# Kernel optimization log

Hardware: AMD Instinct MI355X
Metric: run time of the kernel (lower is better)

The kernel has to match this reference:

```python
import jax, jax.numpy as jnp
import numpy as np

N = 50000      # total nodes (batched protein graphs)
D = 256        # prot_hidden_dim
E = 800000     # edges per relation type
R = 5          # edge types: SEQ, STR_KNN, STR_DIS, SURF, LRR_REGION
LN_EPS = 1e-5
SIGMOID_TEMP = 2.0
WEIGHT_SCALE = 2.0
MIN_W, MAX_W = 0.05, 2.0


def setup_inputs() -> dict:
    key = jax.random.key(0)
    ks = jax.random.split(key, 8)
    x = jax.random.normal(ks[0], (N, D), dtype=jnp.float32)
    src = jax.random.randint(ks[1], (R, E), 0, N)
    dst = jax.random.randint(ks[2], (R, E), 0, N)
    # relation-attention MLP params: Linear(D, D//4) -> LayerNorm(D//4) -> ReLU -> Linear(D//4, 1)
    H = D // 4
    W1 = jax.random.normal(ks[3], (D, H), dtype=jnp.float32) / np.float32(np.sqrt(D))
    b1 = jnp.zeros((H,), jnp.float32)
    gamma = jnp.ones((H,), jnp.float32)
    beta = jnp.zeros((H,), jnp.float32)
    W2 = jax.random.normal(ks[4], (H, 1), dtype=jnp.float32) / np.float32(np.sqrt(H))
    b2 = jnp.zeros((1,), jnp.float32)
    attn_bias = jnp.array([-4.0, -4.0, -4.0, -4.0, -2.772], jnp.float32)
    return {"x": x, "src": src, "dst": dst, "W1": W1, "b1": b1,
            "gamma": gamma, "beta": beta, "W2": W2, "b2": b2,
            "attn_bias": attn_bias}


def _mean_aggregate(x, s, d):
    # DGL update_all(copy_u('h','m'), mean('m','h')): scatter-mean of src feats onto dst.
    sums = jax.ops.segment_sum(x[s], d, num_segments=N)                      # [N, D]
    cnt = jax.ops.segment_sum(jnp.ones((E,), x.dtype), d, num_segments=N)    # [N]
    # zero in-degree nodes get 0 (DGL mean semantics)
    return jnp.where(cnt[:, None] > 0, sums / jnp.maximum(cnt, 1.0)[:, None], 0.0)


def reference(x, src, dst, W1, b1, gamma, beta, W2, b2, attn_bias):
    # per-relation mean aggregation (loop over fixed small R, not a data dim)
    agg = jnp.stack([_mean_aggregate(x, src[r], dst[r]) for r in range(R)])  # [R, N, D]
    g = agg.mean(axis=1)                                                     # [R, D]
    # relation-attention MLP (dropout = identity in eval)
    h = g @ W1 + b1                                                          # [R, D//4]
    mu = h.mean(axis=-1, keepdims=True)
    var = ((h - mu) ** 2).mean(axis=-1, keepdims=True)
    h = (h - mu) * jax.lax.rsqrt(var + LN_EPS) * gamma + beta
    h = jax.nn.relu(h)
    scores = (h @ W2 + b2)[:, 0] + attn_bias                                 # [R]
    w = jax.nn.sigmoid(scores / SIGMOID_TEMP) * WEIGHT_SCALE
    w = jnp.clip(w, MIN_W, MAX_W)
    # fused = sum_r w[r] * agg[r]
    return jnp.einsum('r,rnd->nd', w, agg)
```

## Files before the change

kernel.cpp:

```cpp
#include <hip/hip_runtime.h>

#define NN 50000
#define DD 256
#define EE 800000
#define RR 5
#define HH 64
#define RN (RR * NN)

#define F_OFF  (RN)
#define F_CUR  (2 * RN)
#define F_C    (3 * RN)
#define F_G    (4 * RN)
#define F_W    (4 * RN + 1280)
#define F_CTR  (4 * RN + 1288)
#define F_ESRC (4 * RN + 1296)
#define F_XH   (F_ESRC + RR * EE)
#define BYTES_BF16 ((size_t)(F_XH + NN * DD / 2) * 4)
#define BYTES_F32  ((size_t)(F_ESRC + RR * EE) * 4)

#define C2_OFF  (RN)
#define C2_CUR  (2 * RN)
#define C2_G    (3 * RN)
#define C2_W    (3 * RN + 1280)
#define C2_CTR  (3 * RN + 1288)
#define C2_ESRC (3 * RN + 1296)
#define BYTES_CSR2 ((size_t)(C2_ESRC + RR * EE) * 4)

__device__ inline unsigned short bf16rn(float f) {
    unsigned u = __float_as_uint(f);
    unsigned r = u + 0x7FFFu + ((u >> 16) & 1u);
    return (unsigned short)(r >> 16);
}

__global__ __launch_bounds__(256) void deg_kernel(const int* __restrict__ dst,
                                                  int* __restrict__ cnt) {
    int i = blockIdx.x * 256 + threadIdx.x;
    if (i < RR * EE) {
        int r = i / EE;
        atomicAdd(&cnt[r * NN + dst[i]], 1);
    }
}

__global__ __launch_bounds__(256) void off_kernel(int* cnt, int* __restrict__ off,
                                                  int* __restrict__ cur,
                                                  int* __restrict__ ctr, float* invc) {
    int i = blockIdx.x * 256 + threadIdx.x;
    if (i < RN) {
        int cv = cnt[i];
        int o = atomicAdd(ctr, cv);
        off[i] = o;
        cur[i] = o;
        invc[i] = (cv > 0) ? (1.0f / (float)cv) : 0.0f;
    }
}

template <bool WITH_C>
__global__ __launch_bounds__(256) void fill_kernel(const int* __restrict__ src,
                                                   const int* __restrict__ dst,
                                                   int* __restrict__ cur,
                                                   int* __restrict__ esrc,
                                                   const float* __restrict__ invc,
                                                   float* __restrict__ c) {
    int i = blockIdx.x * 256 + threadIdx.x;
    if (i < RR * EE) {
        int r = i / EE;
        int d = dst[i];
        int s = src[i];
        int slot = atomicAdd(&cur[r * NN + d], 1);
        esrc[slot] = s;
        if constexpr (WITH_C) {
            unsafeAtomicAdd(&c[r * NN + s], invc[r * NN + d]);
        }
    }
}

__global__ __launch_bounds__(256) void gmat_kernel(const float* __restrict__ x,
                                                   const float* __restrict__ c,
                                                   float* __restrict__ g) {
    const int wave = threadIdx.x >> 6;
    const int lane = threadIdx.x & 63;
    const int gw = blockIdx.x * 4 + wave;
    const int nw = gridDim.x * 4;
    float4 a0 = {0, 0, 0, 0}, a1 = {0, 0, 0, 0}, a2 = {0, 0, 0, 0},
           a3 = {0, 0, 0, 0}, a4 = {0, 0, 0, 0};
    for (int s = gw; s < NN; s += nw) {
        float4 v = ((const float4*)(x + (size_t)s * DD))[lane];
        float c0 = c[0 * NN + s], c1 = c[1 * NN + s], c2 = c[2 * NN + s],
              c3 = c[3 * NN + s], c4 = c[4 * NN + s];
        a0.x += c0 * v.x; a0.y += c0 * v.y; a0.z += c0 * v.z; a0.w += c0 * v.w;
        a1.x += c1 * v.x; a1.y += c1 * v.y; a1.z += c1 * v.z; a1.w += c1 * v.w;
        a2.x += c2 * v.x; a2.y += c2 * v.y; a2.z += c2 * v.z; a2.w += c2 * v.w;
        a3.x += c3 * v.x; a3.y += c3 * v.y; a3.z += c3 * v.z; a3.w += c3 * v.w;
        a4.x += c4 * v.x; a4.y += c4 * v.y; a4.z += c4 * v.z; a4.w += c4 * v.w;
    }
    float4 acc[5] = {a0, a1, a2, a3, a4};
    #pragma unroll
    for (int r = 0; r < RR; ++r) {
        float* gr = g + r * DD + lane * 4;
        unsafeAtomicAdd(gr + 0, acc[r].x);
        unsafeAtomicAdd(gr + 1, acc[r].y);
        unsafeAtomicAdd(gr + 2, acc[r].z);
        unsafeAtomicAdd(gr + 3, acc[r].w);
    }
}

__global__ __launch_bounds__(256) void g_kernel(const float* __restrict__ x,
                                                const int* __restrict__ src,
                                                const int* __restrict__ dst,
                                                const float* __restrict__ invc,
                                                float* __restrict__ g) {
    const int r = blockIdx.y;
    const int wave = threadIdx.x >> 6;
    const int lane = threadIdx.x & 63;
    const int gw = blockIdx.x * 4 + wave;
    const int nw = gridDim.x * 4;
    const int* __restrict__ srcR = src + r * EE;
    const int* __restrict__ dstR = dst + r * EE;
    const float* __restrict__ invcR = invc + r * NN;
    float4 acc = {0, 0, 0, 0};
    for (int e = gw; e < EE; e += nw) {
        int eu = __builtin_amdgcn_readfirstlane(e);
        int s = srcR[eu];
        int dn = dstR[eu];
        float ic = invcR[dn];
        float4 v = ((const float4*)(x + (size_t)s * DD))[lane];
        acc.x += v.x * ic; acc.y += v.y * ic; acc.z += v.z * ic; acc.w += v.w * ic;
    }
    float* gr = g + r * DD + lane * 4;
    unsafeAtomicAdd(gr + 0, acc.x);
    unsafeAtomicAdd(gr + 1, acc.y);
    unsafeAtomicAdd(gr + 2, acc.z);
    unsafeAtomicAdd(gr + 3, acc.w);
}

__global__ __launch_bounds__(64) void mlp_kernel(const float* __restrict__ gsum,
                                                 const float* __restrict__ W1,
                                                 const float* __restrict__ b1,
                                                 const float* __restrict__ gamma,
                                                 const float* __restrict__ beta,
                                                 const float* __restrict__ W2,
                                                 const float* __restrict__ b2,
                                                 const float* __restrict__ attn_bias,
                                                 float* __restrict__ w) {
    const int t = threadIdx.x;
    __shared__ float gs[DD];
    const float invN = 1.0f / (float)NN;
    for (int r = 0; r < RR; ++r) {
        for (int d = t; d < DD; d += 64) gs[d] = gsum[r * DD + d] * invN;
        __syncthreads();
        float h = b1[t];
        for (int d = 0; d < DD; ++d) h += gs[d] * W1[d * HH + t];
        float mu = h;
        #pragma unroll
        for (int o = 32; o; o >>= 1) mu += __shfl_xor(mu, o, 64);
        mu *= (1.0f / 64.0f);
        float cc = h - mu;
        float var = cc * cc;
        #pragma unroll
        for (int o = 32; o; o >>= 1) var += __shfl_xor(var, o, 64);
        var *= (1.0f / 64.0f);
        float hn = cc * rsqrtf(var + 1e-5f) * gamma[t] + beta[t];
        hn = fmaxf(hn, 0.0f);
        float sc = hn * W2[t];
        #pragma unroll
        for (int o = 32; o; o >>= 1) sc += __shfl_xor(sc, o, 64);
        if (t == 0) {
            float s = sc + b2[0] + attn_bias[r];
            float ww = 2.0f / (1.0f + expf(-s * 0.5f));
            ww = fminf(fmaxf(ww, 0.05f), 2.0f);
            w[r] = ww;
        }
        __syncthreads();
    }
}

__global__ __launch_bounds__(256) void xcvt_kernel(const float* __restrict__ x,
                                                   ushort4* __restrict__ xh) {
    int i = blockIdx.x * 256 + threadIdx.x;
    if (i < NN * DD / 4) {
        float4 v = ((const float4*)x)[i];
        ushort4 q;
        q.x = bf16rn(v.x); q.y = bf16rn(v.y); q.z = bf16rn(v.z); q.w = bf16rn(v.w);
        xh[i] = q;
    }
}

template <bool BF16>
__device__ inline float4 loadrow(const float* __restrict__ x,
                                 const ushort4* __restrict__ xh, int s, int lane) {
    if constexpr (BF16) {
        ushort4 q = xh[(size_t)s * (DD / 4) + lane];
        float4 v;
        v.x = __uint_as_float((unsigned)q.x << 16);
        v.y = __uint_as_float((unsigned)q.y << 16);
        v.z = __uint_as_float((unsigned)q.z << 16);
        v.w = __uint_as_float((unsigned)q.w << 16);
        return v;
    } else {
        return ((const float4*)(x + (size_t)s * DD))[lane];
    }
}

template <bool BF16>
__global__ __launch_bounds__(256) void out_pull_kernel(const float* __restrict__ x,
                                                       const ushort4* __restrict__ xh,
                                                       const int* __restrict__ esrc,
                                                       const int* __restrict__ off,
                                                       const int* __restrict__ endv,
                                                       const float* __restrict__ invc,
                                                       const float* __restrict__ w,
                                                       float* __restrict__ out) {
    const int node = blockIdx.x * 4 + (threadIdx.x >> 6);
    if (node >= NN) return;
    const int lane = threadIdx.x & 63;

    float4 acc = {0, 0, 0, 0};
    #pragma unroll
    for (int r = 0; r < RR; ++r) {
        const int idx = r * NN + node;
        const int b = __builtin_amdgcn_readfirstlane(off[idx]);
        const int e_ = __builtin_amdgcn_readfirstlane(endv[idx]);
        const float coef = w[r] * invc[idx];
        float4 t = {0, 0, 0, 0};
        int e = b;
        for (; e + 4 <= e_; e += 4) {
            int s0 = __builtin_amdgcn_readfirstlane(esrc[e + 0]);
            int s1 = __builtin_amdgcn_readfirstlane(esrc[e + 1]);
            int s2 = __builtin_amdgcn_readfirstlane(esrc[e + 2]);
            int s3 = __builtin_amdgcn_readfirstlane(esrc[e + 3]);
            float4 v0 = loadrow<BF16>(x, xh, s0, lane);
            float4 v1 = loadrow<BF16>(x, xh, s1, lane);
            float4 v2 = loadrow<BF16>(x, xh, s2, lane);
            float4 v3 = loadrow<BF16>(x, xh, s3, lane);
            t.x += (v0.x + v1.x) + (v2.x + v3.x);
            t.y += (v0.y + v1.y) + (v2.y + v3.y);
            t.z += (v0.z + v1.z) + (v2.z + v3.z);
            t.w += (v0.w + v1.w) + (v2.w + v3.w);
        }
        for (; e < e_; ++e) {
            int s = __builtin_amdgcn_readfirstlane(esrc[e]);
            float4 v = loadrow<BF16>(x, xh, s, lane);
            t.x += v.x; t.y += v.y; t.z += v.z; t.w += v.w;
        }
        acc.x += coef * t.x; acc.y += coef * t.y;
        acc.z += coef * t.z; acc.w += coef * t.w;
    }
    ((float4*)(out + (size_t)node * DD))[lane] = acc;
}

__global__ __launch_bounds__(256) void invcnt_kernel(float* __restrict__ c) {
    int i = blockIdx.x * 256 + threadIdx.x;
    if (i < RN) {
        int v = ((const int*)c)[i];
        c[i] = (v > 0) ? (1.0f / (float)v) : 0.0f;
    }
}

__global__ __launch_bounds__(256) void out_scatter_kernel(const float* __restrict__ x,
                                                          const int* __restrict__ src,
                                                          const int* __restrict__ dst,
                                                          const float* __restrict__ invc,
                                                          const float* __restrict__ w,
                                                          float* __restrict__ out) {
    const int r = blockIdx.y;
    const float wr = w[r];
    const int wave = threadIdx.x >> 6;
    const int lane = threadIdx.x & 63;
    const int gw = blockIdx.x * 4 + wave;
    const int nw = gridDim.x * 4;
    const int* __restrict__ srcR = src + r * EE;
    const int* __restrict__ dstR = dst + r * EE;
    const float* __restrict__ invcR = invc + r * NN;
    for (int e = gw; e < EE; e += nw) {
        int eu = __builtin_amdgcn_readfirstlane(e);
        int s = srcR[eu];
        int dn = dstR[eu];
        float coef = wr * invcR[dn];
        float4 v = ((const float4*)(x + (size_t)s * DD))[lane];
        float* o = out + (size_t)dn * DD + lane * 4;
        unsafeAtomicAdd(o + 0, v.x * coef);
        unsafeAtomicAdd(o + 1, v.y * coef);
        unsafeAtomicAdd(o + 2, v.z * coef);
        unsafeAtomicAdd(o + 3, v.w * coef);
    }
}

extern "C" void kernel_launch(void* const* d_in, const int* in_sizes, int n_in,
                              void* d_out, int out_size, void* d_ws, size_t ws_size,
                              hipStream_t stream) {
    const float* x = (const float*)d_in[0];
    const int* src = (const int*)d_in[1];
    const int* dst = (const int*)d_in[2];
    const float* W1 = (const float*)d_in[3];
    const float* b1 = (const float*)d_in[4];
    const float* gamma = (const float*)d_in[5];
    const float* beta = (const float*)d_in[6];
    const float* W2 = (const float*)d_in[7];
    const float* b2 = (const float*)d_in[8];
    const float* attn_bias = (const float*)d_in[9];
    float* out = (float*)d_out;
    float* ws = (float*)d_ws;

    const int EDGE_GRID = (RR * EE + 255) / 256;
    const int RN_GRID = (RN + 255) / 256;

    if (ws_size >= BYTES_F32) {
        const bool bf16 = (ws_size >= BYTES_BF16);
        int* cnt = (int*)ws;
        float* invc = ws;
        int* off = (int*)ws + F_OFF;
        int* cur = (int*)ws + F_CUR;
        float* c = ws + F_C;
        float* g = ws + F_G;
        float* w = ws + F_W;
        int* ctr = (int*)ws + F_CTR;
        int* esrc = (int*)ws + F_ESRC;
        ushort4* xh = (ushort4*)((int*)ws + F_XH);

        hipMemsetAsync(cnt, 0, (size_t)RN * 4, stream);
        hipMemsetAsync(c, 0, (size_t)(RN + 1296) * 4, stream);

        if (bf16)
            xcvt_kernel<<<(NN * DD / 4 + 255) / 256, 256, 0, stream>>>(x, xh);
        deg_kernel<<<EDGE_GRID, 256, 0, stream>>>(dst, cnt);
        off_kernel<<<RN_GRID, 256, 0, stream>>>(cnt, off, cur, ctr, invc);
        fill_kernel<true><<<EDGE_GRID, 256, 0, stream>>>(src, dst, cur, esrc, invc, c);
        gmat_kernel<<<128, 256, 0, stream>>>(x, c, g);
        mlp_kernel<<<1, 64, 0, stream>>>(g, W1, b1, gamma, beta, W2, b2, attn_bias, w);
        if (bf16)
            out_pull_kernel<true><<<(NN + 3) / 4, 256, 0, stream>>>(x, xh, esrc, off,
                                                                    cur, invc, w, out);
        else
            out_pull_kernel<false><<<(NN + 3) / 4, 256, 0, stream>>>(x, xh, esrc, off,
                                                                     cur, invc, w, out);
    } else if (ws_size >= BYTES_CSR2) {
        int* cnt = (int*)ws;
        float* invc = ws;
        int* off = (int*)ws + C2_OFF;
        int* cur = (int*)ws + C2_CUR;
        float* g = ws + C2_G;
        float* w = ws + C2_W;
        int* ctr = (int*)ws + C2_CTR;
        int* esrc = (int*)ws + C2_ESRC;

        hipMemsetAsync(cnt, 0, (size_t)RN * 4, stream);
        hipMemsetAsync(g, 0, (size_t)1296 * 4, stream);

        deg_kernel<<<EDGE_GRID, 256, 0, stream>>>(dst, cnt);
        off_kernel<<<RN_GRID, 256, 0, stream>>>(cnt, off, cur, ctr, invc);
        fill_kernel<false><<<EDGE_GRID, 256, 0, stream>>>(src, dst, cur, esrc, invc,
                                                          nullptr);
        g_kernel<<<dim3(512, RR), 256, 0, stream>>>(x, src, dst, invc, g);
        mlp_kernel<<<1, 64, 0, stream>>>(g, W1, b1, gamma, beta, W2, b2, attn_bias, w);
        out_pull_kernel<false><<<(NN + 3) / 4, 256, 0, stream>>>(x, nullptr, esrc, off,
                                                                 cur, invc, w, out);
    } else {
        float* cnt = ws;
        float* g = ws + RN;
        float* w = ws + RN + RR * DD;
        hipMemsetAsync(ws, 0, (size_t)(RN + RR * DD + RR) * 4, stream);
        hipMemsetAsync(d_out, 0, (size_t)NN * DD * 4, stream);
        deg_kernel<<<EDGE_GRID, 256, 0, stream>>>(dst, (int*)cnt);
        invcnt_kernel<<<RN_GRID, 256, 0, stream>>>(cnt);
        g_kernel<<<dim3(512, RR), 256, 0, stream>>>(x, src, dst, cnt, g);
        mlp_kernel<<<1, 64, 0, stream>>>(g, W1, b1, gamma, beta, W2, b2, attn_bias, w);
        out_scatter_kernel<<<dim3(512, RR), 256, 0, stream>>>(x, src, dst, cnt, w, out);
    }
}
```

Before: 1.137 ms.

## Rebuild CSR with deterministic ranks, 16-bit indices, and column-chunked bf16 pull

The CSR build now records each edge's rank during the degree count and computes offsets with a block-level prefix scan, so the fill pass needs no atomics on the cursor array. Source indices are stored as 16-bit values, and x is converted to bf16 in a chunked layout of 8 chunks of 32 columns. The output pull then runs once per chunk so each pass gathers from a smaller working set that fits better in cache. The MLP now handles all five relations in one 320-thread block with W1 staged in shared memory. This adds seven more kernel launches and repeats the esrc and offset reads for every chunk, and the 16-bit indices only hold because N is below 65536.

New measurement: 1.434 ms. 26.1% more time.

```diff
diff --git a/kernel.cpp b/kernel.cpp
--- a/kernel.cpp
+++ b/kernel.cpp
@@ -6,17 +6,22 @@
 #define RR 5
 #define HH 64
 #define RN (RR * NN)
-
-#define F_OFF  (RN)
-#define F_CUR  (2 * RN)
-#define F_C    (3 * RN)
-#define F_G    (4 * RN)
-#define F_W    (4 * RN + 1280)
-#define F_CTR  (4 * RN + 1288)
-#define F_ESRC (4 * RN + 1296)
-#define F_XH   (F_ESRC + RR * EE)
-#define BYTES_BF16 ((size_t)(F_XH + NN * DD / 2) * 4)
-#define BYTES_F32  ((size_t)(F_ESRC + RR * EE) * 4)
+#define NBLK ((NN + 255) / 256)
+#define NCHUNK 8
+#define CW 32
+
+typedef float v2f __attribute__((ext_vector_type(2)));
+
+#define Q_OFF   (RN)
+#define Q_C     (2 * RN + 4)
+#define Q_G     (3 * RN + 4)
+#define Q_W     (3 * RN + 1284)
+#define Q_BSUM  (3 * RN + 1292)
+#define Q_BBASE (3 * RN + 1548)
+#define Q_RANK  (3 * RN + 1804)
+#define Q_ESRC  (Q_RANK + RR * EE / 2)
+#define Q_XH    (Q_ESRC + RR * EE / 2)
+#define BYTES_Q ((size_t)(Q_XH + NCHUNK * NN * CW / 2) * 4)
 
 #define C2_OFF  (RN)
 #define C2_CUR  (2 * RN)
@@ -32,45 +37,105 @@
     return (unsigned short)(r >> 16);
 }
 
-__global__ __launch_bounds__(256) void deg_kernel(const int* __restrict__ dst,
-                                                  int* __restrict__ cnt) {
+
+__global__ __launch_bounds__(256) void deg2_kernel(const int* __restrict__ dst,
+                                                   int* __restrict__ cnt,
+                                                   unsigned short* __restrict__ rank) {
     int i = blockIdx.x * 256 + threadIdx.x;
     if (i < RR * EE) {
         int r = i / EE;
-        atomicAdd(&cnt[r * NN + dst[i]], 1);
-    }
-}
-
-__global__ __launch_bounds__(256) void off_kernel(int* cnt, int* __restrict__ off,
-                                                  int* __restrict__ cur,
-                                                  int* __restrict__ ctr, float* invc) {
-    int i = blockIdx.x * 256 + threadIdx.x;
-    if (i < RN) {
-        int cv = cnt[i];
-        int o = atomicAdd(ctr, cv);
-        off[i] = o;
-        cur[i] = o;
-        invc[i] = (cv > 0) ? (1.0f / (float)cv) : 0.0f;
-    }
-}
-
-template <bool WITH_C>
-__global__ __launch_bounds__(256) void fill_kernel(const int* __restrict__ src,
-                                                   const int* __restrict__ dst,
-                                                   int* __restrict__ cur,
-                                                   int* __restrict__ esrc,
-                                                   const float* __restrict__ invc,
-                                                   float* __restrict__ c) {
+        int old = atomicAdd(&cnt[r * NN + dst[i]], 1);
+        rank[i] = (unsigned short)old;
+    }
+}
+
+__global__ __launch_bounds__(256) void bsum_kernel(const int* __restrict__ cnt,
+                                                   int* __restrict__ bsum) {
+    __shared__ int sh[256];
+    const int t = threadIdx.x;
+    const int d = blockIdx.x * 256 + t;
+    int tot = 0;
+    if (d < NN) {
+        #pragma unroll
+        for (int r = 0; r < RR; ++r) tot += cnt[r * NN + d];
+    }
+    sh[t] = tot;
+    __syncthreads();
+    for (int o = 128; o; o >>= 1) {
+        if (t < o) sh[t] += sh[t + o];
+        __syncthreads();
+    }
+    if (t == 0) bsum[blockIdx.x] = sh[0];
+}
+
+__global__ __launch_bounds__(256) void bscan2_kernel(const int* __restrict__ bsum,
+                                                     int* __restrict__ bbase,
+                                                     int* __restrict__ off) {
+    __shared__ int sh[256];
+    const int t = threadIdx.x;
+    int v = (t < NBLK) ? bsum[t] : 0;
+    sh[t] = v;
+    __syncthreads();
+    for (int o = 1; o < 256; o <<= 1) {
+        int p = (t >= o) ? sh[t - o] : 0;
+        __syncthreads();
+        sh[t] += p;
+        __syncthreads();
+    }
+    if (t < NBLK) bbase[t] = sh[t] - v;
+    if (t == 0) off[RN] = RR * EE;
+}
+
+__global__ __launch_bounds__(256) void off3_kernel(int* __restrict__ cnt_invc,
+                                                   const int* __restrict__ bbase,
+                                                   int* __restrict__ off) {
+    __shared__ int sh[256];
+    const int t = threadIdx.x;
+    const int d = blockIdx.x * 256 + t;
+    int cc[RR];
+    int tot = 0;
+    if (d < NN) {
+        #pragma unroll
+        for (int r = 0; r < RR; ++r) {
+            cc[r] = cnt_invc[r * NN + d];
+            tot += cc[r];
+        }
+    }
+    sh[t] = tot;
+    __syncthreads();
+    for (int o = 1; o < 256; o <<= 1) {
+        int p = (t >= o) ? sh[t - o] : 0;
+        __syncthreads();
+        sh[t] += p;
+        __syncthreads();
+    }
+    if (d < NN) {
+        int base = bbase[blockIdx.x] + sh[t] - tot;
+        float* invc = (float*)cnt_invc;
+        #pragma unroll
+        for (int r = 0; r < RR; ++r) {
+            off[d * RR + r] = base;
+            base += cc[r];
+            invc[r * NN + d] = (cc[r] > 0) ? (1.0f / (float)cc[r]) : 0.0f;
+        }
+    }
+}
+
+__global__ __launch_bounds__(256) void fill3_kernel(const int* __restrict__ src,
+                                                    const int* __restrict__ dst,
+                                                    const unsigned short* __restrict__ rank,
+                                                    const int* __restrict__ off,
+                                                    unsigned short* __restrict__ esrc,
+                                                    const float* __restrict__ invc,
+                                                    float* __restrict__ c) {
     int i = blockIdx.x * 256 + threadIdx.x;
     if (i < RR * EE) {
         int r = i / EE;
         int d = dst[i];
         int s = src[i];
-        int slot = atomicAdd(&cur[r * NN + d], 1);
-        esrc[slot] = s;
-        if constexpr (WITH_C) {
-            unsafeAtomicAdd(&c[r * NN + s], invc[r * NN + d]);
-        }
+        int slot = off[d * RR + r] + (int)rank[i];
+        esrc[slot] = (unsigned short)s;
+        unsafeAtomicAdd(&c[r * NN + s], invc[r * NN + d]);
     }
 }
 
@@ -101,6 +166,136 @@
         unsafeAtomicAdd(gr + 1, acc[r].y);
         unsafeAtomicAdd(gr + 2, acc[r].z);
         unsafeAtomicAdd(gr + 3, acc[r].w);
+    }
+}
+
+__global__ __launch_bounds__(320) void mlp5_kernel(const float* __restrict__ gsum,
+                                                   const float* __restrict__ W1,
+                                                   const float* __restrict__ b1,
+                                                   const float* __restrict__ gamma,
+                                                   const float* __restrict__ beta,
+                                                   const float* __restrict__ W2,
+                                                   const float* __restrict__ b2,
+                                                   const float* __restrict__ attn_bias,
+                                                   float* __restrict__ w) {
+    __shared__ float w1s[DD * HH];
+    __shared__ float gss[RR][DD];
+    const int tid = threadIdx.x;
+    for (int k = tid; k < DD * HH; k += 320) w1s[k] = W1[k];
+    const int r = tid >> 6;
+    const int t = tid & 63;
+    for (int d = t; d < DD; d += 64) gss[r][d] = gsum[r * DD + d] * (1.0f / (float)NN);
+    __syncthreads();
+    float h = b1[t];
+    for (int d = 0; d < DD; ++d) h += gss[r][d] * w1s[d * HH + t];
+    float mu = h;
+    #pragma unroll
+    for (int o = 32; o; o >>= 1) mu += __shfl_xor(mu, o, 64);
+    mu *= (1.0f / 64.0f);
+    float cc = h - mu;
+    float var = cc * cc;
+    #pragma unroll
+    for (int o = 32; o; o >>= 1) var += __shfl_xor(var, o, 64);
+    var *= (1.0f / 64.0f);
+    float hn = cc * rsqrtf(var + 1e-5f) * gamma[t] + beta[t];
+    hn = fmaxf(hn, 0.0f);
+    float sc = hn * W2[t];
+    #pragma unroll
+    for (int o = 32; o; o >>= 1) sc += __shfl_xor(sc, o, 64);
+    if (t == 0) {
+        float s = sc + b2[0] + attn_bias[r];
+        float ww = 2.0f / (1.0f + expf(-s * 0.5f));
+        ww = fminf(fmaxf(ww, 0.05f), 2.0f);
+        w[r] = ww;
+    }
+}
+
+__global__ __launch_bounds__(256) void xcvt2_kernel(const float* __restrict__ x,
+                                                    unsigned short* __restrict__ xh2) {
+    int i = blockIdx.x * 256 + threadIdx.x;
+    if (i < NN * DD / 4) {
+        int srow = i >> 6;
+        int q4 = i & 63;
+        float4 v = ((const float4*)x)[i];
+        int chunk = q4 >> 3;
+        int pos = q4 & 7;
+        ushort4 q;
+        q.x = bf16rn(v.x); q.y = bf16rn(v.y); q.z = bf16rn(v.z); q.w = bf16rn(v.w);
+        *(ushort4*)(xh2 + ((size_t)chunk * NN + srow) * CW + pos * 4) = q;
+    }
+}
+
+__global__ __launch_bounds__(256) void pullc_kernel(const unsigned short* __restrict__ xh2,
+                                                    const unsigned short* __restrict__ esrc,
+                                                    const int* __restrict__ off,
+                                                    const float* __restrict__ invc,
+                                                    const float* __restrict__ w,
+                                                    float* __restrict__ out,
+                                                    int chunk) {
+    const int node = blockIdx.x * 4 + (threadIdx.x >> 6);
+    if (node >= NN) return;
+    const int lane = threadIdx.x & 63;
+    const int grp = lane >> 4;
+    const int sl = lane & 15;
+    const ushort2* __restrict__ xc =
+        (const ushort2*)(xh2 + (size_t)chunk * NN * CW);
+    float ax = 0.0f, ay = 0.0f;
+    #pragma unroll
+    for (int r = 0; r < RR; ++r) {
+        const int idx = node * RR + r;
+        const int b = __builtin_amdgcn_readfirstlane(off[idx]);
+        const int e_ = __builtin_amdgcn_readfirstlane(off[idx + 1]);
+        const float coef = w[r] * invc[r * NN + node];
+        float tx = 0.0f, ty = 0.0f;
+        for (int e = b + grp; e < e_; e += 4) {
+            int s = (int)__builtin_nontemporal_load(&esrc[e]);
+            ushort2 q = xc[s * 16 + sl];
+            tx += __uint_as_float((unsigned)q.x << 16);
+            ty += __uint_as_float((unsigned)q.y << 16);
+        }
+        ax += coef * tx;
+        ay += coef * ty;
+    }
+    ax += __shfl_xor(ax, 16, 64); ax += __shfl_xor(ax, 32, 64);
+    ay += __shfl_xor(ay, 16, 64); ay += __shfl_xor(ay, 32, 64);
+    if (grp == 0) {
+        v2f v = {ax, ay};
+        __builtin_nontemporal_store(
+            v, (v2f*)(out + (size_t)node * DD + chunk * CW + sl * 2));
+    }
+}
+
+__global__ __launch_bounds__(256) void deg_kernel(const int* __restrict__ dst,
+                                                  int* __restrict__ cnt) {
+    int i = blockIdx.x * 256 + threadIdx.x;
+    if (i < RR * EE) {
+        int r = i / EE;
+        atomicAdd(&cnt[r * NN + dst[i]], 1);
+    }
+}
+
+__global__ __launch_bounds__(256) void off_kernel(int* cnt, int* __restrict__ off,
+                                                  int* __restrict__ cur,
+                                                  int* __restrict__ ctr, float* invc) {
+    int i = blockIdx.x * 256 + threadIdx.x;
+    if (i < RN) {
+        int cv = cnt[i];
+        int o = atomicAdd(ctr, cv);
+        off[i] = o;
+        cur[i] = o;
+        invc[i] = (cv > 0) ? (1.0f / (float)cv) : 0.0f;
+    }
+}
+
+__global__ __launch_bounds__(256) void fill_kernel(const int* __restrict__ src,
+                                                   const int* __restrict__ dst,
+                                                   int* __restrict__ cur,
+                                                   int* __restrict__ esrc) {
+    int i = blockIdx.x * 256 + threadIdx.x;
+    if (i < RR * EE) {
+        int r = i / EE;
+        int slot = atomicAdd(&cur[r * NN + dst[i]], 1);
+        esrc[slot] = src[i];
     }
 }
 
@@ -133,77 +328,7 @@
     unsafeAtomicAdd(gr + 3, acc.w);
 }
 
-__global__ __launch_bounds__(64) void mlp_kernel(const float* __restrict__ gsum,
-                                                 const float* __restrict__ W1,
-                                                 const float* __restrict__ b1,
-                                                 const float* __restrict__ gamma,
-                                                 const float* __restrict__ beta,
-                                                 const float* __restrict__ W2,
-                                                 const float* __restrict__ b2,
-                                                 const float* __restrict__ attn_bias,
-                                                 float* __restrict__ w) {
-    const int t = threadIdx.x;
-    __shared__ float gs[DD];
-    const float invN = 1.0f / (float)NN;
-    for (int r = 0; r < RR; ++r) {
-        for (int d = t; d < DD; d += 64) gs[d] = gsum[r * DD + d] * invN;
-        __syncthreads();
-        float h = b1[t];
-        for (int d = 0; d < DD; ++d) h += gs[d] * W1[d * HH + t];
-        float mu = h;
-        #pragma unroll
-        for (int o = 32; o; o >>= 1) mu += __shfl_xor(mu, o, 64);
-        mu *= (1.0f / 64.0f);
-        float cc = h - mu;
-        float var = cc * cc;
-        #pragma unroll
-        for (int o = 32; o; o >>= 1) var += __shfl_xor(var, o, 64);
-        var *= (1.0f / 64.0f);
-        float hn = cc * rsqrtf(var + 1e-5f) * gamma[t] + beta[t];
-        hn = fmaxf(hn, 0.0f);
-        float sc = hn * W2[t];
-        #pragma unroll
-        for (int o = 32; o; o >>= 1) sc += __shfl_xor(sc, o, 64);
-        if (t == 0) {
-            float s = sc + b2[0] + attn_bias[r];
-            float ww = 2.0f / (1.0f + expf(-s * 0.5f));
-            ww = fminf(fmaxf(ww, 0.05f), 2.0f);
-            w[r] = ww;
-        }
-        __syncthreads();
-    }
-}
-
-__global__ __launch_bounds__(256) void xcvt_kernel(const float* __restrict__ x,
-                                                   ushort4* __restrict__ xh) {
-    int i = blockIdx.x * 256 + threadIdx.x;
-    if (i < NN * DD / 4) {
-        float4 v = ((const float4*)x)[i];
-        ushort4 q;
-        q.x = bf16rn(v.x); q.y = bf16rn(v.y); q.z = bf16rn(v.z); q.w = bf16rn(v.w);
-        xh[i] = q;
-    }
-}
-
-template <bool BF16>
-__device__ inline float4 loadrow(const float* __restrict__ x,
-                                 const ushort4* __restrict__ xh, int s, int lane) {
-    if constexpr (BF16) {
-        ushort4 q = xh[(size_t)s * (DD / 4) + lane];
-        float4 v;
-        v.x = __uint_as_float((unsigned)q.x << 16);
-        v.y = __uint_as_float((unsigned)q.y << 16);
-        v.z = __uint_as_float((unsigned)q.z << 16);
-        v.w = __uint_as_float((unsigned)q.w << 16);
-        return v;
-    } else {
-        return ((const float4*)(x + (size_t)s * DD))[lane];
-    }
-}
-
-template <bool BF16>
 __global__ __launch_bounds__(256) void out_pull_kernel(const float* __restrict__ x,
-                                                       const ushort4* __restrict__ xh,
                                                        const int* __restrict__ esrc,
                                                        const int* __restrict__ off,
                                                        const int* __restrict__ endv,
@@ -213,7 +338,6 @@
     const int node = blockIdx.x * 4 + (threadIdx.x >> 6);
     if (node >= NN) return;
     const int lane = threadIdx.x & 63;
-
     float4 acc = {0, 0, 0, 0};
     #pragma unroll
     for (int r = 0; r < RR; ++r) {
@@ -222,24 +346,9 @@
         const int e_ = __builtin_amdgcn_readfirstlane(endv[idx]);
         const float coef = w[r] * invc[idx];
         float4 t = {0, 0, 0, 0};
-        int e = b;
-        for (; e + 4 <= e_; e += 4) {
-            int s0 = __builtin_amdgcn_readfirstlane(esrc[e + 0]);
-            int s1 = __builtin_amdgcn_readfirstlane(esrc[e + 1]);
-            int s2 = __builtin_amdgcn_readfirstlane(esrc[e + 2]);
-            int s3 = __builtin_amdgcn_readfirstlane(esrc[e + 3]);
-            float4 v0 = loadrow<BF16>(x, xh, s0, lane);
-            float4 v1 = loadrow<BF16>(x, xh, s1, lane);
-            float4 v2 = loadrow<BF16>(x, xh, s2, lane);
-            float4 v3 = loadrow<BF16>(x, xh, s3, lane);
-            t.x += (v0.x + v1.x) + (v2.x + v3.x);
-            t.y += (v0.y + v1.y) + (v2.y + v3.y);
-            t.z += (v0.z + v1.z) + (v2.z + v3.z);
-            t.w += (v0.w + v1.w) + (v2.w + v3.w);
-        }
-        for (; e < e_; ++e) {
+        for (int e = b; e < e_; ++e) {
             int s = __builtin_amdgcn_readfirstlane(esrc[e]);
-            float4 v = loadrow<BF16>(x, xh, s, lane);
+            float4 v = ((const float4*)(x + (size_t)s * DD))[lane];
             t.x += v.x; t.y += v.y; t.z += v.z; t.w += v.w;
         }
         acc.x += coef * t.x; acc.y += coef * t.y;
@@ -304,35 +413,33 @@
     const int EDGE_GRID = (RR * EE + 255) / 256;
     const int RN_GRID = (RN + 255) / 256;
 
-    if (ws_size >= BYTES_F32) {
-        const bool bf16 = (ws_size >= BYTES_BF16);
+    if (ws_size >= BYTES_Q) {
         int* cnt = (int*)ws;
         float* invc = ws;
-        int* off = (int*)ws + F_OFF;
-        int* cur = (int*)ws + F_CUR;
-        float* c = ws + F_C;
-        float* g = ws + F_G;
-        float* w = ws + F_W;
-        int* ctr = (int*)ws + F_CTR;
-        int* esrc = (int*)ws + F_ESRC;
-        ushort4* xh = (ushort4*)((int*)ws + F_XH);
+        int* off = (int*)ws + Q_OFF;
+        float* c = ws + Q_C;
+        float* g = ws + Q_G;
+        float* w = ws + Q_W;
+        int* bsum = (int*)ws + Q_BSUM;
+        int* bbase = (int*)ws + Q_BBASE;
+        unsigned short* rank = (unsigned short*)((int*)ws + Q_RANK);
+        unsigned short* esrc = (unsigned short*)((int*)ws + Q_ESRC);
+        unsigned short* xh2 = (unsigned short*)((int*)ws + Q_XH);
 
         hipMemsetAsync(cnt, 0, (size_t)RN * 4, stream);
-        hipMemsetAsync(c, 0, (size_t)(RN + 1296) * 4, stream);
-
-        if (bf16)
-            xcvt_kernel<<<(NN * DD / 4 + 255) / 256, 256, 0, stream>>>(x, xh);
-        deg_kernel<<<EDGE_GRID, 256, 0, stream>>>(dst, cnt);
-        off_kernel<<<RN_GRID, 256, 0, stream>>>(cnt, off, cur, ctr, invc);
-        fill_kernel<true><<<EDGE_GRID, 256, 0, stream>>>(src, dst, cur, esrc, invc, c);
+        hipMemsetAsync(c, 0, (size_t)(RN + 1288) * 4, stream);
+
+        xcvt2_kernel<<<(NN * DD / 4 + 255) / 256, 256, 0, stream>>>(x, xh2);
+        deg2_kernel<<<EDGE_GRID, 256, 0, stream>>>(dst, cnt, rank);
+        bsum_kernel<<<NBLK, 256, 0, stream>>>(cnt, bsum);
+        bscan2_kernel<<<1, 256, 0, stream>>>(bsum, bbase, off);
+        off3_kernel<<<NBLK, 256, 0, stream>>>(cnt, bbase, off);
+        fill3_kernel<<<EDGE_GRID, 256, 0, stream>>>(src, dst, rank, off, esrc, invc, c);
         gmat_kernel<<<128, 256, 0, stream>>>(x, c, g);
-        mlp_kernel<<<1, 64, 0, stream>>>(g, W1, b1, gamma, beta, W2, b2, attn_bias, w);
-        if (bf16)
-            out_pull_kernel<true><<<(NN + 3) / 4, 256, 0, stream>>>(x, xh, esrc, off,
-                                                                    cur, invc, w, out);
-        else
-            out_pull_kernel<false><<<(NN + 3) / 4, 256, 0, stream>>>(x, xh, esrc, off,
-                                                                     cur, invc, w, out);
+        mlp5_kernel<<<1, 320, 0, stream>>>(g, W1, b1, gamma, beta, W2, b2, attn_bias, w);
+        for (int chunk = 0; chunk < NCHUNK; ++chunk)
+            pullc_kernel<<<(NN + 3) / 4, 256, 0, stream>>>(xh2, esrc, off, invc, w,
+                                                           out, chunk);
     } else if (ws_size >= BYTES_CSR2) {
         int* cnt = (int*)ws;
         float* invc = ws;
@@ -348,12 +455,11 @@
 
         deg_kernel<<<EDGE_GRID, 256, 0, stream>>>(dst, cnt);
         off_kernel<<<RN_GRID, 256, 0, stream>>>(cnt, off, cur, ctr, invc);
-        fill_kernel<false><<<EDGE_GRID, 256, 0, stream>>>(src, dst, cur, esrc, invc,
-                                                          nullptr);
+        fill_kernel<<<EDGE_GRID, 256, 0, stream>>>(src, dst, cur, esrc);
         g_kernel<<<dim3(512, RR), 256, 0, stream>>>(x, src, dst, invc, g);
-        mlp_kernel<<<1, 64, 0, stream>>>(g, W1, b1, gamma, beta, W2, b2, attn_bias, w);
-        out_pull_kernel<false><<<(NN + 3) / 4, 256, 0, stream>>>(x, nullptr, esrc, off,
-                                                                 cur, invc, w, out);
+        mlp5_kernel<<<1, 320, 0, stream>>>(g, W1, b1, gamma, beta, W2, b2, attn_bias, w);
+        out_pull_kernel<<<(NN + 3) / 4, 256, 0, stream>>>(x, esrc, off, cur, invc, w,
+                                                          out);
     } else {
         float* cnt = ws;
         float* g = ws + RN;
@@ -363,7 +469,7 @@
         deg_kernel<<<EDGE_GRID, 256, 0, stream>>>(dst, (int*)cnt);
         invcnt_kernel<<<RN_GRID, 256, 0, stream>>>(cnt);
         g_kernel<<<dim3(512, RR), 256, 0, stream>>>(x, src, dst, cnt, g);
-        mlp_kernel<<<1, 64, 0, stream>>>(g, W1, b1, gamma, beta, W2, b2, attn_bias, w);
+        mlp5_kernel<<<1, 320, 0, stream>>>(g, W1, b1, gamma, beta, W2, b2, attn_bias, w);
         out_scatter_kernel<<<dim3(512, RR), 256, 0, stream>>>(x, src, dst, cnt, w, out);
     }
 }
```
